# Kernel tuning notes

Measured on AMD Instinct MI355X. Metric: run time of the kernel, lower is better.

The kernel has to match this reference:

```python
import jax, jax.numpy as jnp
import numpy as np

OUT_FEATURES = 8192
IN_FEATURES = 8192
BATCH = 512


def setup_inputs() -> dict:
    key = jax.random.key(0)
    k_x, k_w, k_s = jax.random.split(key, 3)
    x = jax.random.normal(k_x, (BATCH, IN_FEATURES), dtype=jnp.float32)
    # packed int4 weights: each int holds two nibbles (values 0..255)
    packed_weight = jax.random.randint(k_w, (OUT_FEATURES, IN_FEATURES // 2), 0, 256, dtype=jnp.int32)
    # per-output-row scale (positive, as produced by abs-max quantization)
    scale = jax.random.uniform(k_s, (OUT_FEATURES, 1), dtype=jnp.float32) * 0.02 + 1e-4
    return {"x": x, "packed_weight": packed_weight, "scale": scale}


def reference(x, packed_weight, scale):
    # Unpack two 4-bit values per byte: high nibble first (matches torch loop:
    # col i <- packed >> 4 & 15, col i+1 <- packed & 15), then subtract zero-point 8.
    hi = (packed_weight >> 4) & 15
    lo = packed_weight & 15
    q = jnp.stack([hi, lo], axis=-1).reshape(OUT_FEATURES, IN_FEATURES) - 8  # [out, in] int
    w = q.astype(scale.dtype) * scale  # dequantized weight [out, in]
    # linear: y = x @ W^T
    return jnp.einsum('bi,oi->bo', x, w)
```

## Files before the change

### kernel.cpp

```cpp
#include <hip/hip_runtime.h>
#include <cstdint>
#include <cstddef>

#define IN_F 8192
#define OUT_F 8192
#define BATCH 512
#define KSPLIT 4
#define KSLICE (IN_F / KSPLIT)
#define BK 32
#define NIT (KSLICE / BK)

typedef __bf16 bf16x8 __attribute__((ext_vector_type(8)));
typedef float floatx4 __attribute__((ext_vector_type(4)));

__device__ __forceinline__ ushort f2bf(float f) {
  uint32_t u = __float_as_uint(f);
  u += 0x7FFFu + ((u >> 16) & 1u);
  return (ushort)(u >> 16);
}

__device__ __forceinline__ uint32_t dq(int p) {
  uint32_t u = (uint32_t)p;
  return (((u >> 4) & 0xFu) | ((u & 0xFu) << 16)) | 0x43004300u;
}

__global__ __launch_bounds__(256) void cvt_rowsum(const float* __restrict__ x,
                                                  ushort* __restrict__ xb,
                                                  float* __restrict__ rowsum) {
  const int b = blockIdx.x;
  const int t = threadIdx.x;
  const float4* xr = (const float4*)(x + (size_t)b * IN_F);
  ushort4* xo = (ushort4*)(xb + (size_t)b * IN_F);
  float s[4] = {0.f, 0.f, 0.f, 0.f};
#pragma unroll
  for (int i = 0; i < 8; ++i) {
    float4 v = xr[i * 256 + t];
    ushort4 o;
    o.x = f2bf(v.x); o.y = f2bf(v.y); o.z = f2bf(v.z); o.w = f2bf(v.w);
    xo[i * 256 + t] = o;
    s[i >> 1] += __uint_as_float((uint32_t)o.x << 16) + __uint_as_float((uint32_t)o.y << 16)
               + __uint_as_float((uint32_t)o.z << 16) + __uint_as_float((uint32_t)o.w << 16);
  }
  __shared__ float red[4][4];
  const int lane = t & 63, wid = t >> 6;
#pragma unroll
  for (int j = 0; j < 4; ++j) {
    float v = s[j];
#pragma unroll
    for (int off = 32; off >= 1; off >>= 1) v += __shfl_down(v, off, 64);
    if (lane == 0) red[wid][j] = v;
  }
  __syncthreads();
  if (t < 4) rowsum[t * BATCH + b] = red[0][t] + red[1][t] + red[2][t] + red[3][t];
}

__global__ __launch_bounds__(256, 2) void qgemm(const ushort* __restrict__ xb,
                                                const int* __restrict__ pw,
                                                const float* __restrict__ scale,
                                                const float* __restrict__ rowsum,
                                                float* __restrict__ out) {
  __shared__ uint32_t As[2 * 128 * 16];
  __shared__ uint32_t Bs[2 * 128 * 16];

  const int tid = threadIdx.x;
  const int lane = tid & 63;
  const int w = tid >> 6;
  const int wm = w & 1, wn = w >> 1;
  const int lr = lane & 15, lq = lane >> 4;

  const int n0 = blockIdx.x * 128;
  const int m0 = blockIdx.y * 128;
  const int ks = blockIdx.z;

  const int r = tid >> 1, h = tid & 1;
  const char* aG = (const char*)xb + (size_t)(m0 + r) * (IN_F * 2) + ks * (KSLICE * 2) + h * 32;
  const char* bG = (const char*)pw + (size_t)(n0 + r) * (IN_F * 2) + ks * (KSLICE * 2) + h * 32;

  uint32_t* aW = As + r * 16 + h * 8;
  uint32_t* bW = Bs + r * 16 + h * 8;
  const uint32_t* aR = As + (wm * 64 + lr) * 16 + lq * 4;
  const uint32_t* bR = Bs + (wn * 64 + lr) * 16 + lq * 4;

  floatx4 acc[4][4] = {};

  int4 pa0 = *(const int4*)(aG);
  int4 pa1 = *(const int4*)(aG + 16);
  int4 pb0 = *(const int4*)(bG);
  int4 pb1 = *(const int4*)(bG + 16);
  aG += 64; bG += 64;

  for (int it = 0; it < NIT; ++it) {
    const int off = (it & 1) * (128 * 16);
    *(int4*)(aW + off) = pa0;
    *(int4*)(aW + off + 4) = pa1;
    int4 u0, u1;
    u0.x = dq(pb0.x); u0.y = dq(pb0.y); u0.z = dq(pb0.z); u0.w = dq(pb0.w);
    u1.x = dq(pb1.x); u1.y = dq(pb1.y); u1.z = dq(pb1.z); u1.w = dq(pb1.w);
    *(int4*)(bW + off) = u0;
    *(int4*)(bW + off + 4) = u1;
    __syncthreads();
    if (it + 1 < NIT) {
      pa0 = *(const int4*)(aG);
      pa1 = *(const int4*)(aG + 16);
      pb0 = *(const int4*)(bG);
      pb1 = *(const int4*)(bG + 16);
      aG += 64; bG += 64;
    }
    bf16x8 av[4], bv[4];
#pragma unroll
    for (int i = 0; i < 4; ++i) av[i] = *(const bf16x8*)(aR + off + i * 256);
#pragma unroll
    for (int i = 0; i < 4; ++i) bv[i] = *(const bf16x8*)(bR + off + i * 256);
#pragma unroll
    for (int mi = 0; mi < 4; ++mi)
#pragma unroll
      for (int ni = 0; ni < 4; ++ni)
        acc[mi][ni] = __builtin_amdgcn_mfma_f32_16x16x32_bf16(av[mi], bv[ni],
                                                              acc[mi][ni], 0, 0, 0);
  }

  const int om = m0 + wm * 64 + lq * 4;
  const int on = n0 + wn * 64 + lr;
  float scv[4];
#pragma unroll
  for (int ni = 0; ni < 4; ++ni) scv[ni] = scale[on + ni * 16];
  float rsv[4][4];
#pragma unroll
  for (int mi = 0; mi < 4; ++mi)
#pragma unroll
    for (int rr = 0; rr < 4; ++rr)
      rsv[mi][rr] = rowsum[ks * BATCH + om + mi * 16 + rr];

#pragma unroll
  for (int mi = 0; mi < 4; ++mi)
#pragma unroll
    for (int ni = 0; ni < 4; ++ni) {
      const float s = scv[ni];
      float* op = out + (size_t)(om + mi * 16) * OUT_F + (on + ni * 16);
#pragma unroll
      for (int rr = 0; rr < 4; ++rr)
        atomicAdd(op + (size_t)rr * OUT_F, s * (acc[mi][ni][rr] - 136.f * rsv[mi][rr]));
    }
}

extern "C" void kernel_launch(void* const* d_in, const int* in_sizes, int n_in,
                              void* d_out, int out_size, void* d_ws, size_t ws_size,
                              hipStream_t stream) {
  const float* x = (const float*)d_in[0];
  const int* pw = (const int*)d_in[1];
  const float* scale = (const float*)d_in[2];
  float* out = (float*)d_out;

  ushort* xb = (ushort*)d_ws;
  float* rowsum = (float*)((char*)d_ws + (size_t)BATCH * IN_F * sizeof(ushort));

  cvt_rowsum<<<BATCH, 256, 0, stream>>>(x, xb, rowsum);
  hipMemsetAsync(out, 0, (size_t)out_size * sizeof(float), stream);
  dim3 grid(OUT_F / 128, BATCH / 128, KSPLIT);
  qgemm<<<grid, 256, 0, stream>>>(xb, pw, scale, rowsum, out);
}
```

Measured before the change: 309.6 us.

## Widen N tile to 256, load A via global_load_lds, swizzle LDS

Doubles the output-column tile per block to 256, so each warp computes a 64x128 sub-tile and A data is reused across more MFMAs. Activation tiles are now copied straight from global memory into LDS with global_load_lds instead of passing through registers. Both A and B tiles use an XOR swizzle on the 16-byte column index to reduce LDS bank conflicts. In exchange, accumulator registers double, which may lower occupancy or cause spills, and the grid has half as many blocks.

```diff
diff --git a/kernel.cpp b/kernel.cpp
--- a/kernel.cpp
+++ b/kernel.cpp
@@ -9,6 +9,8 @@
 #define KSLICE (IN_F / KSPLIT)
 #define BK 32
 #define NIT (KSLICE / BK)
+#define BM 128
+#define BN 256
 
 typedef __bf16 bf16x8 __attribute__((ext_vector_type(8)));
 typedef float floatx4 __attribute__((ext_vector_type(4)));
@@ -22,6 +24,12 @@
 __device__ __forceinline__ uint32_t dq(int p) {
   uint32_t u = (uint32_t)p;
   return (((u >> 4) & 0xFu) | ((u & 0xFu) << 16)) | 0x43004300u;
+}
+
+__device__ __forceinline__ void gl16(const void* g, uint32_t* l) {
+  __builtin_amdgcn_global_load_lds(
+      (const __attribute__((address_space(1))) uint32_t*)g,
+      (__attribute__((address_space(3))) uint32_t*)l, 16, 0, 0);
 }
 
 __global__ __launch_bounds__(256) void cvt_rowsum(const float* __restrict__ x,
@@ -59,8 +67,8 @@
                                                 const float* __restrict__ scale,
                                                 const float* __restrict__ rowsum,
                                                 float* __restrict__ out) {
-  __shared__ uint32_t As[2 * 128 * 16];
-  __shared__ uint32_t Bs[2 * 128 * 16];
+  __shared__ uint32_t As[2 * BM * 16];
+  __shared__ uint32_t Bs[2 * BN * 16];
 
   const int tid = threadIdx.x;
   const int lane = tid & 63;
@@ -68,62 +76,69 @@
   const int wm = w & 1, wn = w >> 1;
   const int lr = lane & 15, lq = lane >> 4;
 
-  const int n0 = blockIdx.x * 128;
-  const int m0 = blockIdx.y * 128;
+  const int n0 = blockIdx.x * BN;
+  const int m0 = blockIdx.y * BM;
   const int ks = blockIdx.z;
 
-  const int r = tid >> 1, h = tid & 1;
-  const char* aG = (const char*)xb + (size_t)(m0 + r) * (IN_F * 2) + ks * (KSLICE * 2) + h * 32;
-  const char* bG = (const char*)pw + (size_t)(n0 + r) * (IN_F * 2) + ks * (KSLICE * 2) + h * 32;
+  const int qsw = (lane & 3) ^ ((lane >> 3) & 3);
+  const char* aG = (const char*)xb
+      + (size_t)(m0 + w * 32 + (lane >> 2)) * (IN_F * 2)
+      + (size_t)ks * (KSLICE * 2) + qsw * 16;
+  uint32_t* aL = As + (w * 32) * 16;
 
-  uint32_t* aW = As + r * 16 + h * 8;
-  uint32_t* bW = Bs + r * 16 + h * 8;
-  const uint32_t* aR = As + (wm * 64 + lr) * 16 + lq * 4;
-  const uint32_t* bR = Bs + (wn * 64 + lr) * 16 + lq * 4;
+  const int4* bG = (const int4*)(pw + (size_t)(n0 + tid) * (IN_F / 2) + ks * (KSLICE / 2));
+  uint32_t* bW = Bs + tid * 16;
+  const int bkey = (tid >> 1) & 3;
 
-  floatx4 acc[4][4] = {};
+  const int rkey = (lr >> 1) & 3;
+  const uint32_t* aR = As + (wm * 64 + lr) * 16 + (lq ^ rkey) * 4;
+  const uint32_t* bR = Bs + (wn * 128 + lr) * 16 + (lq ^ rkey) * 4;
 
-  int4 pa0 = *(const int4*)(aG);
-  int4 pa1 = *(const int4*)(aG + 16);
-  int4 pb0 = *(const int4*)(bG);
-  int4 pb1 = *(const int4*)(bG + 16);
-  aG += 64; bG += 64;
+  floatx4 acc[4][8] = {};
+
+  gl16(aG, aL);
+  gl16(aG + (size_t)16 * (IN_F * 2), aL + 256);
+  int4 pb0 = bG[0], pb1 = bG[1], pb2 = bG[2], pb3 = bG[3];
 
   for (int it = 0; it < NIT; ++it) {
-    const int off = (it & 1) * (128 * 16);
-    *(int4*)(aW + off) = pa0;
-    *(int4*)(aW + off + 4) = pa1;
-    int4 u0, u1;
+    const int offA = (it & 1) * (BM * 16);
+    const int offB = (it & 1) * (BN * 16);
+    int4 u0, u1, u2, u3;
     u0.x = dq(pb0.x); u0.y = dq(pb0.y); u0.z = dq(pb0.z); u0.w = dq(pb0.w);
     u1.x = dq(pb1.x); u1.y = dq(pb1.y); u1.z = dq(pb1.z); u1.w = dq(pb1.w);
-    *(int4*)(bW + off) = u0;
-    *(int4*)(bW + off + 4) = u1;
+    u2.x = dq(pb2.x); u2.y = dq(pb2.y); u2.z = dq(pb2.z); u2.w = dq(pb2.w);
+    u3.x = dq(pb3.x); u3.y = dq(pb3.y); u3.z = dq(pb3.z); u3.w = dq(pb3.w);
+    *(int4*)(bW + offB + ((0 ^ bkey) << 2)) = u0;
+    *(int4*)(bW + offB + ((1 ^ bkey) << 2)) = u1;
+    *(int4*)(bW + offB + ((2 ^ bkey) << 2)) = u2;
+    *(int4*)(bW + offB + ((3 ^ bkey) << 2)) = u3;
     __syncthreads();
     if (it + 1 < NIT) {
-      pa0 = *(const int4*)(aG);
-      pa1 = *(const int4*)(aG + 16);
-      pb0 = *(const int4*)(bG);
-      pb1 = *(const int4*)(bG + 16);
-      aG += 64; bG += 64;
+      const int offA2 = ((it + 1) & 1) * (BM * 16);
+      const char* aN = aG + (size_t)(it + 1) * 64;
+      gl16(aN, aL + offA2);
+      gl16(aN + (size_t)16 * (IN_F * 2), aL + offA2 + 256);
+      pb0 = bG[(it + 1) * 4 + 0]; pb1 = bG[(it + 1) * 4 + 1];
+      pb2 = bG[(it + 1) * 4 + 2]; pb3 = bG[(it + 1) * 4 + 3];
     }
-    bf16x8 av[4], bv[4];
+    bf16x8 av[4], bv[8];
 #pragma unroll
-    for (int i = 0; i < 4; ++i) av[i] = *(const bf16x8*)(aR + off + i * 256);
+    for (int i = 0; i < 4; ++i) av[i] = *(const bf16x8*)(aR + offA + i * 256);
 #pragma unroll
-    for (int i = 0; i < 4; ++i) bv[i] = *(const bf16x8*)(bR + off + i * 256);
+    for (int i = 0; i < 8; ++i) bv[i] = *(const bf16x8*)(bR + offB + i * 256);
 #pragma unroll
     for (int mi = 0; mi < 4; ++mi)
 #pragma unroll
-      for (int ni = 0; ni < 4; ++ni)
+      for (int ni = 0; ni < 8; ++ni)
         acc[mi][ni] = __builtin_amdgcn_mfma_f32_16x16x32_bf16(av[mi], bv[ni],
                                                               acc[mi][ni], 0, 0, 0);
   }
 
   const int om = m0 + wm * 64 + lq * 4;
-  const int on = n0 + wn * 64 + lr;
-  float scv[4];
+  const int on = n0 + wn * 128 + lr;
+  float scv[8];
 #pragma unroll
-  for (int ni = 0; ni < 4; ++ni) scv[ni] = scale[on + ni * 16];
+  for (int ni = 0; ni < 8; ++ni) scv[ni] = scale[on + ni * 16];
   float rsv[4][4];
 #pragma unroll
   for (int mi = 0; mi < 4; ++mi)
@@ -134,7 +149,7 @@
 #pragma unroll
   for (int mi = 0; mi < 4; ++mi)
 #pragma unroll
-    for (int ni = 0; ni < 4; ++ni) {
+    for (int ni = 0; ni < 8; ++ni) {
       const float s = scv[ni];
       float* op = out + (size_t)(om + mi * 16) * OUT_F + (on + ni * 16);
 #pragma unroll
@@ -156,6 +171,6 @@
 
   cvt_rowsum<<<BATCH, 256, 0, stream>>>(x, xb, rowsum);
   hipMemsetAsync(out, 0, (size_t)out_size * sizeof(float), stream);
-  dim3 grid(OUT_F / 128, BATCH / 128, KSPLIT);
+  dim3 grid(OUT_F / BN, BATCH / BM, KSPLIT);
   qgemm<<<grid, 256, 0, stream>>>(xb, pw, scale, rowsum, out);
 }
```

After: 339.8 us. +9.8%, slower.
